# Optimization experiments

Measured on AMD Instinct MI355X. Metric: run time of the kernel, lower is better.

Reference implementation:

```python
import jax, jax.numpy as jnp
import numpy as np

HIDDEN = 2048
N_HEADS = 16
N_KV_HEADS = 4
HEAD_DIM = 128
N_REP = N_HEADS // N_KV_HEADS
BATCH = 2
SEQ = 2048
SCALE = HEAD_DIM ** -0.5
NEG = -1e9


def apply_rope(x, freqs):
    # x: (b, s, h, d); freqs: (s, d//2) angles. Interleaved-pair rotation.
    cos = jnp.cos(freqs)[None, :, None, :]
    sin = jnp.sin(freqs)[None, :, None, :]
    x1 = x[..., 0::2]
    x2 = x[..., 1::2]
    r1 = x1 * cos - x2 * sin
    r2 = x1 * sin + x2 * cos
    return jnp.stack([r1, r2], axis=-1).reshape(x.shape)


def setup_inputs() -> dict:
    key = jax.random.key(0)
    ks = jax.random.split(key, 6)
    x = jax.random.normal(ks[0], (BATCH, SEQ, HIDDEN), dtype=jnp.float32)
    wq = jax.random.normal(ks[1], (N_HEADS * HEAD_DIM, HIDDEN), dtype=jnp.float32) * 0.02
    wk = jax.random.normal(ks[2], (N_KV_HEADS * HEAD_DIM, HIDDEN), dtype=jnp.float32) * 0.02
    wv = jax.random.normal(ks[3], (N_KV_HEADS * HEAD_DIM, HIDDEN), dtype=jnp.float32) * 0.02
    wo = jax.random.normal(ks[4], (HIDDEN, N_HEADS * HEAD_DIM), dtype=jnp.float32) * 0.02
    # RoPE angle table: pos * theta^{-2i/d}
    inv_freq = 1.0 / (10000.0 ** (jnp.arange(0, HEAD_DIM, 2, dtype=jnp.float32) / HEAD_DIM))
    rope_freqs = jnp.arange(SEQ, dtype=jnp.float32)[:, None] * inv_freq[None, :]  # (S, d/2)
    # additive causal mask
    causal = jnp.tril(jnp.ones((SEQ, SEQ), dtype=bool))
    mask = jnp.where(causal, 0.0, NEG).astype(jnp.float32)[None, None]  # (1,1,S,S)
    return {"x": x, "wq": wq, "wk": wk, "wv": wv, "wo": wo,
            "rope_freqs": rope_freqs, "mask": mask}


def reference(x, wq, wk, wv, wo, rope_freqs, mask):
    b, s, _ = x.shape
    q = (x @ wq.T).reshape(b, s, N_HEADS, HEAD_DIM)
    k = (x @ wk.T).reshape(b, s, N_KV_HEADS, HEAD_DIM)
    v = (x @ wv.T).reshape(b, s, N_KV_HEADS, HEAD_DIM)
    q = apply_rope(q, rope_freqs)
    k = apply_rope(k, rope_freqs)
    new_k, new_v = k, v  # kv cache (no prior cache, start_pos=0)
    # GQA: repeat each kv head n_rep times (matches expand+reshape in source)
    k_rep = jnp.repeat(k, N_REP, axis=2)  # (b, s, n_heads, d)
    v_rep = jnp.repeat(v, N_REP, axis=2)
    scores = jnp.einsum('bqhd,bkhd->bhqk', q, k_rep) * SCALE
    scores = scores + mask
    attn = jax.nn.softmax(scores.astype(jnp.float32), axis=-1).astype(q.dtype)
    out = jnp.einsum('bhqk,bkhd->bqhd', attn, v_rep).reshape(b, s, -1)
    return out @ wo.T, (new_k, new_v)
```

## Files before the change

### kernel.cpp

```cpp
#include <hip/hip_runtime.h>
#include <hip/hip_bf16.h>

#define NH 16
#define NKV 4
#define HD 128
#define QSCALE 0.1275174272f

using bf16x8 = __attribute__((ext_vector_type(8))) __bf16;
using f32x4  = __attribute__((ext_vector_type(4))) float;
using u16x8  = __attribute__((ext_vector_type(8))) unsigned short;
using u16x4  = __attribute__((ext_vector_type(4))) unsigned short;
using u16x2  = __attribute__((ext_vector_type(2))) unsigned short;

__device__ __forceinline__ unsigned short f2b(float f) {
  __hip_bfloat16 h = __float2bfloat16(f);
  return __builtin_bit_cast(unsigned short, h);
}
__device__ __forceinline__ float b2f(unsigned short u) {
  unsigned int v = ((unsigned int)u) << 16;
  return __builtin_bit_cast(float, v);
}

__device__ __forceinline__ void glds16(const unsigned short* g, unsigned short* l) {
  __builtin_amdgcn_global_load_lds(
      (const __attribute__((address_space(1))) unsigned int*)(const void*)g,
      (__attribute__((address_space(3))) unsigned int*)(void*)l, 16, 0, 0);
}

__global__ __launch_bounds__(256) void cvt_fused(const float* __restrict__ x,
                                                 const float* __restrict__ wq,
                                                 const float* __restrict__ wk,
                                                 const float* __restrict__ wv,
                                                 const float* __restrict__ wo,
                                                 const float* __restrict__ freqs,
                                                 unsigned short* __restrict__ xb,
                                                 unsigned short* __restrict__ wqkvb,
                                                 unsigned short* __restrict__ wob,
                                                 float2* __restrict__ cs_tab) {
  int i = blockIdx.x * 256 + threadIdx.x;
  if (i >= 2359296) {
    int k = i - 2359296;
    float f = freqs[k];
    float2 cs; cs.x = cosf(f); cs.y = sinf(f);
    cs_tab[k] = cs;
    return;
  }
  const float* src;
  unsigned short* dst;
  int off;
  if (i < 1048576)      { src = x;  dst = xb;              off = i; }
  else if (i < 1572864) { src = wq; dst = wqkvb;           off = i - 1048576; }
  else if (i < 1703936) { src = wk; dst = wqkvb + 4194304; off = i - 1572864; }
  else if (i < 1835008) { src = wv; dst = wqkvb + 5242880; off = i - 1703936; }
  else                  { src = wo; dst = wob;             off = i - 1835008; }
  const float4* s4 = reinterpret_cast<const float4*>(src) + (size_t)off * 2;
  float4 v0 = s4[0], v1 = s4[1];
  u16x8 o;
  o[0] = f2b(v0.x); o[1] = f2b(v0.y); o[2] = f2b(v0.z); o[3] = f2b(v0.w);
  o[4] = f2b(v1.x); o[5] = f2b(v1.y); o[6] = f2b(v1.z); o[7] = f2b(v1.w);
  reinterpret_cast<u16x8*>(dst)[off] = o;
}


#define GEMM97_PREAMBLE(Kvar)                                                  \
  const int tid = threadIdx.x, lane = tid & 63;                                \
  const int wid = tid >> 6, wm = wid >> 1, wn = wid & 1;                       \
  const int cpx = gridDim.x >> 3;                                              \
  const int wgid = (blockIdx.x & 7) * cpx + (blockIdx.x >> 3);                 \
  const int bx = wgid % nbx, by = wgid / nbx;                                  \
  const int row0 = by * 128, col0 = bx * 128;                                  \
  const int fr = lane & 15, g = lane >> 4;                                     \
  const int NT = (Kvar) >> 5;                                                  \
  size_t offA[2], offB[2];                                                     \
  _Pragma("unroll")                                                            \
  for (int l = 0; l < 2; l++) {                                                \
    int cid = tid + l * 256, R = cid >> 3, phys = cid & 7, cl = phys ^ (R & 7);\
    offA[l] = (size_t)(row0 + 2 * R + (cl >> 2)) * (Kvar) + (cl & 3) * 8;      \
    offB[l] = (size_t)(col0 + 2 * R + (cl >> 2)) * (Kvar) + (cl & 3) * 8;      \
  }

__device__ __forceinline__ bf16x8 ldfrag97(const unsigned short* buf, int row, int g) {
  int R = row >> 1;
  int phys = ((((row & 1) << 2) | g) ^ (R & 7));
  return *reinterpret_cast<const bf16x8*>(&buf[R * 64 + phys * 8]);
}

__global__ __launch_bounds__(256, 3) void gemm_qkv(const unsigned short* __restrict__ A,
                                                   const unsigned short* __restrict__ B,
                                                   const float2* __restrict__ cs_tab,
                                                   unsigned short* __restrict__ qro,
                                                   unsigned short* __restrict__ kro,
                                                   unsigned short* __restrict__ vt,
                                                   float* __restrict__ newk,
                                                   float* __restrict__ newv,
                                                   int K, int nbx) {
  __shared__ unsigned short As[2][128 * 32];
  __shared__ unsigned short Bs[2][128 * 32];
  GEMM97_PREAMBLE(K)

  auto stage = [&](int t, int sb) {
    int k0 = t * 32;
#pragma unroll
    for (int l = 0; l < 2; l++) {
      glds16(A + offA[l] + k0, &As[sb][(tid + l * 256) * 8]);
      glds16(B + offB[l] + k0, &Bs[sb][(tid + l * 256) * 8]);
    }
  };

  f32x4 acc[4][4];
#pragma unroll
  for (int i = 0; i < 4; i++)
#pragma unroll
    for (int j = 0; j < 4; j++) acc[i][j] = f32x4{0.f, 0.f, 0.f, 0.f};

  stage(0, 0);
  int buf = 0;
#pragma unroll 1
  for (int t = 0; t < NT; ++t) {
    __syncthreads();
    if (t + 1 < NT) stage(t + 1, buf ^ 1);
    bf16x8 af[4], bfr[4];
#pragma unroll
    for (int mf = 0; mf < 4; mf++) af[mf] = ldfrag97(As[buf], wm * 64 + mf * 16 + fr, g);
#pragma unroll
    for (int nf = 0; nf < 4; nf++) bfr[nf] = ldfrag97(Bs[buf], wn * 64 + nf * 16 + fr, g);
    __builtin_amdgcn_s_setprio(1);
#pragma unroll
    for (int mf = 0; mf < 4; mf++)
#pragma unroll
      for (int nf = 0; nf < 4; nf++)
        acc[mf][nf] = __builtin_amdgcn_mfma_f32_16x16x32_bf16(af[mf], bfr[nf], acc[mf][nf], 0, 0, 0);
    __builtin_amdgcn_s_setprio(0);
    buf ^= 1;
  }

#pragma unroll
  for (int i = 0; i < 4; i++) {
    int rbase = row0 + wm * 64 + i * 16 + g * 4;
    int bb = rbase >> 11;
    int sr0 = rbase & 2047;
#pragma unroll
    for (int j = 0; j < 4; j++) {
      int cb = col0 + wn * 64 + j * 16 + fr;
      int d = cb & 127;
      if (cb < 2048) {
        int hq = cb >> 7;
        unsigned short* qp = qro + ((size_t)(bb * 16 + hq) * 2048 + sr0) * 128 + d;
#pragma unroll
        for (int r = 0; r < 4; r++) {
          float own = acc[i][j][r];
          float par = __shfl_xor(own, 1);
          float2 cs = cs_tab[(sr0 + r) * 64 + (d >> 1)];
          float o = (fr & 1) ? (par * cs.y + own * cs.x) : (own * cs.x - par * cs.y);
          qp[(size_t)r * 128] = f2b(o * QSCALE);
        }
      } else if (cb < 2560) {
        int kvh = (cb >> 7) & 3;
        unsigned short* kp = kro + ((size_t)(bb * 4 + kvh) * 2048 + sr0) * 128 + d;
        float* nk = newk + ((size_t)bb * 2048 + sr0) * 512 + kvh * 128 + d;
#pragma unroll
        for (int r = 0; r < 4; r++) {
          float own = acc[i][j][r];
          float par = __shfl_xor(own, 1);
          float2 cs = cs_tab[(sr0 + r) * 64 + (d >> 1)];
          float o = (fr & 1) ? (par * cs.y + own * cs.x) : (own * cs.x - par * cs.y);
          kp[(size_t)r * 128] = f2b(o);
          nk[(size_t)r * 512] = o;
        }
      } else {
        int kvh = (cb >> 7) & 3;
        float* nv = newv + ((size_t)bb * 2048 + sr0) * 512 + kvh * 128 + d;
        u16x4 pack;
#pragma unroll
        for (int r = 0; r < 4; r++) {
          float v = acc[i][j][r];
          nv[(size_t)r * 512] = v;
          pack[r] = f2b(v);
        }
        int kl = sr0 & 31;
        int slotb = ((kl >> 2) & 3) * 8 + (kl >> 4) * 4;
        *reinterpret_cast<u16x4*>(vt + ((size_t)(bb * 4 + kvh) * 128 + d) * 2048
                                  + (sr0 & ~31) + slotb) = pack;
      }
    }
  }
}

__global__ __launch_bounds__(256, 3) void gemm_o(const unsigned short* __restrict__ A,
                                                 const unsigned short* __restrict__ B,
                                                 float* __restrict__ C,
                                                 int N, int K, int nbx) {
  __shared__ unsigned short As[2][128 * 32];
  __shared__ unsigned short Bs[2][128 * 32];
  GEMM97_PREAMBLE(K)

  auto stage = [&](int t, int sb) {
    int k0 = t * 32;
#pragma unroll
    for (int l = 0; l < 2; l++) {
      glds16(A + offA[l] + k0, &As[sb][(tid + l * 256) * 8]);
      glds16(B + offB[l] + k0, &Bs[sb][(tid + l * 256) * 8]);
    }
  };

  f32x4 acc[4][4];
#pragma unroll
  for (int i = 0; i < 4; i++)
#pragma unroll
    for (int j = 0; j < 4; j++) acc[i][j] = f32x4{0.f, 0.f, 0.f, 0.f};

  stage(0, 0);
  int buf = 0;
#pragma unroll 1
  for (int t = 0; t < NT; ++t) {
    __syncthreads();
    if (t + 1 < NT) stage(t + 1, buf ^ 1);
    bf16x8 af[4], bfr[4];
#pragma unroll
    for (int mf = 0; mf < 4; mf++) af[mf] = ldfrag97(As[buf], wm * 64 + mf * 16 + fr, g);
#pragma unroll
    for (int nf = 0; nf < 4; nf++) bfr[nf] = ldfrag97(Bs[buf], wn * 64 + nf * 16 + fr, g);
    __builtin_amdgcn_s_setprio(1);
#pragma unroll
    for (int mf = 0; mf < 4; mf++)
#pragma unroll
      for (int nf = 0; nf < 4; nf++)
        acc[mf][nf] = __builtin_amdgcn_mfma_f32_16x16x32_bf16(af[mf], bfr[nf], acc[mf][nf], 0, 0, 0);
    __builtin_amdgcn_s_setprio(0);
    buf ^= 1;
  }

#pragma unroll
  for (int i = 0; i < 4; i++) {
#pragma unroll
    for (int j = 0; j < 4; j++) {
      int rbase = row0 + wm * 64 + i * 16 + g * 4;
      int cb = col0 + wn * 64 + j * 16 + fr;
#pragma unroll
      for (int r = 0; r < 4; r++)
        C[(size_t)(rbase + r) * N + cb] = acc[i][j][r];
    }
  }
}

__global__ __launch_bounds__(512, 4) void attn_kernel(const unsigned short* __restrict__ qro,
                                                      const unsigned short* __restrict__ kro,
                                                      const unsigned short* __restrict__ vt,
                                                      unsigned short* __restrict__ out) {
  __shared__ unsigned short Ks[2][32 * 128];
  __shared__ unsigned short Vs[2][64 * 64];
  const int tid = threadIdx.x, lane = tid & 63, w = tid >> 6;
  const int kvhb = blockIdx.x & 7;
  const int kvh = kvhb & 3, b = kvhb >> 2;
  const int s = blockIdx.x >> 3;
  const int T = (s < 32) ? s : (95 - s);
  const int sub = w >> 2, hh = w & 3;
  const int h = kvh * 4 + hh;
  const int qbase = T * 32 + sub * 16;
  const int fr = lane & 15, g = lane >> 4, fk = g * 8;
  const unsigned short* Kp = kro + (size_t)(b * 4 + kvh) * 2048 * 128;
  const unsigned short* Vtp = vt + (size_t)(b * 4 + kvh) * 128 * 2048;
  const unsigned short* Qp = qro + ((size_t)(b * 16 + h) * 2048 + qbase) * 128;

  bf16x8 qf[4];
#pragma unroll
  for (int kk = 0; kk < 4; kk++)
    qf[kk] = *reinterpret_cast<const bf16x8*>(Qp + fr * 128 + kk * 32 + fk);

  u16x8 onesu;
#pragma unroll
  for (int j = 0; j < 8; j++) onesu[j] = 0x3F80;
  bf16x8 ones = __builtin_bit_cast(bf16x8, onesu);

  f32x4 o[8];
#pragma unroll
  for (int dt = 0; dt < 8; dt++) o[dt] = f32x4{0.f, 0.f, 0.f, 0.f};
  f32x4 dacc = f32x4{0.f, 0.f, 0.f, 0.f};
  const int qrow_s = qbase + fr;
  const int niter = T + 1;

  const int krow = w * 4 + (lane >> 4);
  const int kcol = lane & 15;
  const int vr = w * 8 + (lane >> 3);
  const int vcol = lane & 7;

  auto stage = [&](int kv0, int buf) {
    glds16(Kp + (size_t)(kv0 + krow) * 128 + ((kcol ^ (krow & 7)) * 8),
           &Ks[buf][w * 4 * 128]);
    int u = vcol ^ (vr & 7);
    int d = 2 * vr + (u >> 2);
    glds16(Vtp + (size_t)d * 2048 + kv0 + (u & 3) * 8,
           &Vs[buf][w * 8 * 64]);
  };

  auto step = [&](int kv0, bool mask, int buf) {
    const unsigned short* Kb = &Ks[buf][0];
    const unsigned short* Vb = &Vs[buf][0];
    f32x4 sc[2];
    sc[0] = sc[1] = f32x4{0.f, 0.f, 0.f, 0.f};
    __builtin_amdgcn_s_setprio(1);
#pragma unroll
    for (int kk = 0; kk < 4; kk++) {
      int blk = ((kk * 4 + g) ^ (fr & 7)) * 8;
      bf16x8 ka0 = *reinterpret_cast<const bf16x8*>(Kb + (fr +  0) * 128 + blk);
      bf16x8 ka1 = *reinterpret_cast<const bf16x8*>(Kb + (fr + 16) * 128 + blk);
      sc[0] = __builtin_amdgcn_mfma_f32_16x16x32_bf16(ka0, qf[kk], sc[0], 0, 0, 0);
      sc[1] = __builtin_amdgcn_mfma_f32_16x16x32_bf16(ka1, qf[kk], sc[1], 0, 0, 0);
    }
    __builtin_amdgcn_s_setprio(0);
#pragma unroll
    for (int ss = 0; ss < 2; ss++)
#pragma unroll
      for (int r = 0; r < 4; r++) {
        float v = sc[ss][r];
        if (mask && (kv0 + 16 * ss + 4 * g + r > qrow_s)) v = -1e30f;
        sc[ss][r] = __builtin_amdgcn_exp2f(v);
      }
    u16x8 pau;
#pragma unroll
    for (int j = 0; j < 4; j++) {
      pau[j]     = f2b(sc[0][j]);
      pau[4 + j] = f2b(sc[1][j]);
    }
    bf16x8 pa = __builtin_bit_cast(bf16x8, pau);
    dacc = __builtin_amdgcn_mfma_f32_16x16x32_bf16(pa, ones, dacc, 0, 0, 0);
    __builtin_amdgcn_s_setprio(1);
#pragma unroll
    for (int dt = 0; dt < 8; dt++) {
      int jr = dt * 8 + (fr >> 1);
      int c = ((fr & 1) * 4 + g) ^ (fr >> 1);
      bf16x8 vf = *reinterpret_cast<const bf16x8*>(Vb + jr * 64 + c * 8);
      o[dt] = __builtin_amdgcn_mfma_f32_16x16x32_bf16(pa, vf, o[dt], 0, 0, 0);
    }
    __builtin_amdgcn_s_setprio(0);
  };

  stage(0, 0);
  int buf = 0;
  for (int i = 0; i < niter; i++) {
    __syncthreads();
    if (i + 1 < niter) stage((i + 1) * 32, buf ^ 1);
    step(i * 32, i == niter - 1, buf);
    buf ^= 1;
  }

#pragma unroll
  for (int r = 0; r < 4; r++) {
    float inv = 1.0f / dacc[r];
    int qrow = qbase + g * 4 + r;
    size_t rowoff = ((size_t)b * 2048 + qrow) * 2048 + (size_t)h * 128;
#pragma unroll
    for (int dt = 0; dt < 8; dt++)
      out[rowoff + dt * 16 + fr] = f2b(o[dt][r] * inv);
  }
}

extern "C" void kernel_launch(void* const* d_in, const int* in_sizes, int n_in,
                              void* d_out, int out_size, void* d_ws, size_t ws_size,
                              hipStream_t stream) {
  const float* x  = (const float*)d_in[0];
  const float* wq = (const float*)d_in[1];
  const float* wk = (const float*)d_in[2];
  const float* wv = (const float*)d_in[3];
  const float* wo = (const float*)d_in[4];
  const float* freqs = (const float*)d_in[5];

  char* ws = (char*)d_ws;
  unsigned short* xb    = (unsigned short*)(ws);
  unsigned short* attn  = xb;
  unsigned short* wqkvb = (unsigned short*)(ws + 16777216);
  unsigned short* wob   = (unsigned short*)(ws + 29360128);
  float2*         cstab = (float2*)(ws + 37748736);
  unsigned short* qro   = (unsigned short*)(ws + 62914560);
  unsigned short* kro   = (unsigned short*)(ws + 79691776);
  unsigned short* vt    = (unsigned short*)(ws + 83886080);

  float* out_o = (float*)d_out;
  float* out_k = (float*)d_out + 8388608;
  float* out_v = (float*)d_out + 10485760;

  cvt_fused<<<9728, 256, 0, stream>>>(x, wq, wk, wv, wo, freqs, xb, wqkvb, wob, cstab);

  gemm_qkv<<<768, 256, 0, stream>>>(xb, wqkvb, cstab, qro, kro, vt, out_k, out_v, 2048, 24);

  attn_kernel<<<512, 512, 0, stream>>>(qro, kro, vt, attn);

  gemm_o<<<512, 256, 0, stream>>>(attn, wob, out_o, 2048, 2048, 16);
}
```

Measured before the change: 193.1 us.

## Process two query heads per wave in attention to reuse K/V fragments

Halves the attention block from 8 to 4 waves, with each wave now handling two GQA heads that share the same KV head. Each K and V LDS fragment load then feeds two MFMAs, and each thread issues two staging loads per tile instead of one. The aim is to cut LDS read traffic per MFMA and raise instruction-level parallelism. The cost is roughly double the accumulator registers per wave (launch bounds change to 256 threads, 3 blocks) and fewer waves per block, which may lower occupancy and latency hiding.

```diff
diff --git a/kernel.cpp b/kernel.cpp
--- a/kernel.cpp
+++ b/kernel.cpp
@@ -61,7 +61,6 @@
   reinterpret_cast<u16x8*>(dst)[off] = o;
 }
 
-
 #define GEMM97_PREAMBLE(Kvar)                                                  \
   const int tid = threadIdx.x, lane = tid & 63;                                \
   const int wid = tid >> 6, wm = wid >> 1, wn = wid & 1;                       \
@@ -243,7 +242,7 @@
   }
 }
 
-__global__ __launch_bounds__(512, 4) void attn_kernel(const unsigned short* __restrict__ qro,
+__global__ __launch_bounds__(256, 3) void attn_kernel(const unsigned short* __restrict__ qro,
                                                       const unsigned short* __restrict__ kro,
                                                       const unsigned short* __restrict__ vt,
                                                       unsigned short* __restrict__ out) {
@@ -254,83 +253,107 @@
   const int kvh = kvhb & 3, b = kvhb >> 2;
   const int s = blockIdx.x >> 3;
   const int T = (s < 32) ? s : (95 - s);
-  const int sub = w >> 2, hh = w & 3;
-  const int h = kvh * 4 + hh;
+  const int sub = w >> 1, hp = w & 1;
+  const int h0 = kvh * 4 + hp * 2;
   const int qbase = T * 32 + sub * 16;
   const int fr = lane & 15, g = lane >> 4, fk = g * 8;
   const unsigned short* Kp = kro + (size_t)(b * 4 + kvh) * 2048 * 128;
   const unsigned short* Vtp = vt + (size_t)(b * 4 + kvh) * 128 * 2048;
-  const unsigned short* Qp = qro + ((size_t)(b * 16 + h) * 2048 + qbase) * 128;
-
-  bf16x8 qf[4];
-#pragma unroll
-  for (int kk = 0; kk < 4; kk++)
-    qf[kk] = *reinterpret_cast<const bf16x8*>(Qp + fr * 128 + kk * 32 + fk);
+  const unsigned short* Qp0 = qro + ((size_t)(b * 16 + h0) * 2048 + qbase) * 128;
+  const unsigned short* Qp1 = qro + ((size_t)(b * 16 + h0 + 1) * 2048 + qbase) * 128;
+
+  bf16x8 qf0[4], qf1[4];
+#pragma unroll
+  for (int kk = 0; kk < 4; kk++) {
+    qf0[kk] = *reinterpret_cast<const bf16x8*>(Qp0 + fr * 128 + kk * 32 + fk);
+    qf1[kk] = *reinterpret_cast<const bf16x8*>(Qp1 + fr * 128 + kk * 32 + fk);
+  }
 
   u16x8 onesu;
 #pragma unroll
   for (int j = 0; j < 8; j++) onesu[j] = 0x3F80;
   bf16x8 ones = __builtin_bit_cast(bf16x8, onesu);
 
-  f32x4 o[8];
-#pragma unroll
-  for (int dt = 0; dt < 8; dt++) o[dt] = f32x4{0.f, 0.f, 0.f, 0.f};
-  f32x4 dacc = f32x4{0.f, 0.f, 0.f, 0.f};
+  f32x4 o0[8], o1[8];
+#pragma unroll
+  for (int dt = 0; dt < 8; dt++) { o0[dt] = f32x4{0.f,0.f,0.f,0.f}; o1[dt] = f32x4{0.f,0.f,0.f,0.f}; }
+  f32x4 dacc0 = f32x4{0.f,0.f,0.f,0.f};
+  f32x4 dacc1 = f32x4{0.f,0.f,0.f,0.f};
   const int qrow_s = qbase + fr;
   const int niter = T + 1;
 
-  const int krow = w * 4 + (lane >> 4);
+  const int krow = w * 8 + (lane >> 4);
   const int kcol = lane & 15;
-  const int vr = w * 8 + (lane >> 3);
+  const int vrow = w * 16 + (lane >> 3);
   const int vcol = lane & 7;
 
   auto stage = [&](int kv0, int buf) {
-    glds16(Kp + (size_t)(kv0 + krow) * 128 + ((kcol ^ (krow & 7)) * 8),
-           &Ks[buf][w * 4 * 128]);
-    int u = vcol ^ (vr & 7);
-    int d = 2 * vr + (u >> 2);
-    glds16(Vtp + (size_t)d * 2048 + kv0 + (u & 3) * 8,
-           &Vs[buf][w * 8 * 64]);
+    unsigned short* Kb = &Ks[buf][0];
+    unsigned short* Vb = &Vs[buf][0];
+#pragma unroll
+    for (int j = 0; j < 2; j++) {
+      int r = krow + j * 4;
+      glds16(Kp + (size_t)(kv0 + r) * 128 + ((kcol ^ (r & 7)) * 8),
+             Kb + (w * 8 + j * 4) * 128);
+    }
+#pragma unroll
+    for (int j = 0; j < 2; j++) {
+      int r = vrow + j * 8;
+      int u = vcol ^ (r & 7);
+      int d = 2 * r + (u >> 2);
+      glds16(Vtp + (size_t)d * 2048 + kv0 + (u & 3) * 8,
+             Vb + (w * 16 + j * 8) * 64);
+    }
   };
 
   auto step = [&](int kv0, bool mask, int buf) {
     const unsigned short* Kb = &Ks[buf][0];
     const unsigned short* Vb = &Vs[buf][0];
-    f32x4 sc[2];
-    sc[0] = sc[1] = f32x4{0.f, 0.f, 0.f, 0.f};
+    f32x4 sc0[2], sc1[2];
+    sc0[0] = sc0[1] = f32x4{0.f,0.f,0.f,0.f};
+    sc1[0] = sc1[1] = f32x4{0.f,0.f,0.f,0.f};
     __builtin_amdgcn_s_setprio(1);
 #pragma unroll
     for (int kk = 0; kk < 4; kk++) {
       int blk = ((kk * 4 + g) ^ (fr & 7)) * 8;
       bf16x8 ka0 = *reinterpret_cast<const bf16x8*>(Kb + (fr +  0) * 128 + blk);
       bf16x8 ka1 = *reinterpret_cast<const bf16x8*>(Kb + (fr + 16) * 128 + blk);
-      sc[0] = __builtin_amdgcn_mfma_f32_16x16x32_bf16(ka0, qf[kk], sc[0], 0, 0, 0);
-      sc[1] = __builtin_amdgcn_mfma_f32_16x16x32_bf16(ka1, qf[kk], sc[1], 0, 0, 0);
+      sc0[0] = __builtin_amdgcn_mfma_f32_16x16x32_bf16(ka0, qf0[kk], sc0[0], 0, 0, 0);
+      sc1[0] = __builtin_amdgcn_mfma_f32_16x16x32_bf16(ka0, qf1[kk], sc1[0], 0, 0, 0);
+      sc0[1] = __builtin_amdgcn_mfma_f32_16x16x32_bf16(ka1, qf0[kk], sc0[1], 0, 0, 0);
+      sc1[1] = __builtin_amdgcn_mfma_f32_16x16x32_bf16(ka1, qf1[kk], sc1[1], 0, 0, 0);
     }
     __builtin_amdgcn_s_setprio(0);
 #pragma unroll
     for (int ss = 0; ss < 2; ss++)
 #pragma unroll
       for (int r = 0; r < 4; r++) {
-        float v = sc[ss][r];
-        if (mask && (kv0 + 16 * ss + 4 * g + r > qrow_s)) v = -1e30f;
-        sc[ss][r] = __builtin_amdgcn_exp2f(v);
+        bool m = mask && (kv0 + 16 * ss + 4 * g + r > qrow_s);
+        float v0 = m ? -1e30f : sc0[ss][r];
+        float v1 = m ? -1e30f : sc1[ss][r];
+        sc0[ss][r] = __builtin_amdgcn_exp2f(v0);
+        sc1[ss][r] = __builtin_amdgcn_exp2f(v1);
       }
-    u16x8 pau;
+    u16x8 pau, pbu;
 #pragma unroll
     for (int j = 0; j < 4; j++) {
-      pau[j]     = f2b(sc[0][j]);
-      pau[4 + j] = f2b(sc[1][j]);
+      pau[j]     = f2b(sc0[0][j]);
+      pau[4 + j] = f2b(sc0[1][j]);
+      pbu[j]     = f2b(sc1[0][j]);
+      pbu[4 + j] = f2b(sc1[1][j]);
     }
     bf16x8 pa = __builtin_bit_cast(bf16x8, pau);
-    dacc = __builtin_amdgcn_mfma_f32_16x16x32_bf16(pa, ones, dacc, 0, 0, 0);
+    bf16x8 pb = __builtin_bit_cast(bf16x8, pbu);
+    dacc0 = __builtin_amdgcn_mfma_f32_16x16x32_bf16(pa, ones, dacc0, 0, 0, 0);
+    dacc1 = __builtin_amdgcn_mfma_f32_16x16x32_bf16(pb, ones, dacc1, 0, 0, 0);
     __builtin_amdgcn_s_setprio(1);
 #pragma unroll
     for (int dt = 0; dt < 8; dt++) {
       int jr = dt * 8 + (fr >> 1);
       int c = ((fr & 1) * 4 + g) ^ (fr >> 1);
       bf16x8 vf = *reinterpret_cast<const bf16x8*>(Vb + jr * 64 + c * 8);
-      o[dt] = __builtin_amdgcn_mfma_f32_16x16x32_bf16(pa, vf, o[dt], 0, 0, 0);
+      o0[dt] = __builtin_amdgcn_mfma_f32_16x16x32_bf16(pa, vf, o0[dt], 0, 0, 0);
+      o1[dt] = __builtin_amdgcn_mfma_f32_16x16x32_bf16(pb, vf, o1[dt], 0, 0, 0);
     }
     __builtin_amdgcn_s_setprio(0);
   };
@@ -346,12 +369,15 @@
 
 #pragma unroll
   for (int r = 0; r < 4; r++) {
-    float inv = 1.0f / dacc[r];
+    float inv0 = 1.0f / dacc0[r];
+    float inv1 = 1.0f / dacc1[r];
     int qrow = qbase + g * 4 + r;
-    size_t rowoff = ((size_t)b * 2048 + qrow) * 2048 + (size_t)h * 128;
-#pragma unroll
-    for (int dt = 0; dt < 8; dt++)
-      out[rowoff + dt * 16 + fr] = f2b(o[dt][r] * inv);
+    size_t ro0 = ((size_t)b * 2048 + qrow) * 2048 + (size_t)h0 * 128;
+#pragma unroll
+    for (int dt = 0; dt < 8; dt++) {
+      out[ro0 + dt * 16 + fr]       = f2b(o0[dt][r] * inv0);
+      out[ro0 + 128 + dt * 16 + fr] = f2b(o1[dt][r] * inv1);
+    }
   }
 }
 
@@ -383,7 +409,7 @@
 
   gemm_qkv<<<768, 256, 0, stream>>>(xb, wqkvb, cstab, qro, kro, vt, out_k, out_v, 2048, 24);
 
-  attn_kernel<<<512, 512, 0, stream>>>(qro, kro, vt, attn);
+  attn_kernel<<<512, 256, 0, stream>>>(qro, kro, vt, attn);
 
   gemm_o<<<512, 256, 0, stream>>>(attn, wob, out_o, 2048, 2048, 16);
 }
```

Result: slower. 197.3 us (+2.2%).
